# Kernel tuning notes

Hardware: AMD Instinct MI355X
Metric: run time of the kernel (lower is better)

The kernel has to match this reference:

```python
import jax, jax.numpy as jnp
import numpy as np

NUM_PROJS = 7
BLOCK = 256       # HyperAttention block_size
SAMPLE = 256      # HyperAttention sample_size
NUM_HEADS = 16

def _hamming_perm(n):
    a = np.array([0, 1])
    for _ in range(n - 1):
        a = np.concatenate([a, a[::-1] + a.max() + 1])
    return a

_PERM = jnp.asarray(_hamming_perm(NUM_PROJS))           # [128] gray-code-ish bucket reorder
_ENC = (2 ** jnp.arange(NUM_PROJS)).astype(jnp.int32)   # [7]

def _lsh_hash(mat, proj_dir):
    # mat: [B,H,N,d], proj_dir: [d,7] -> bucket ids [B,H,N]
    bits = jnp.einsum('bhnd,dr->bhnr', mat, proj_dir) > 0
    ids = (bits * _ENC).sum(-1)
    return _PERM[ids]

def _attn_lse(q, k, v, scale, bias=None):
    s = jnp.einsum('...qd,...kd->...qk', q, k) * scale
    if bias is not None:
        s = s + bias
    lse = jax.nn.logsumexp(s, axis=-1, keepdims=True)
    o = jnp.einsum('...qk,...kd->...qd', jnp.exp(s - lse), v)
    return o, lse

def _gather(t, idx):
    # gather rows along axis 2: out[b,h,s] = t[b,h,idx[b,h,s]]
    return jnp.take_along_axis(t, idx[..., None], axis=2)

def setup_inputs():
    key = jax.random.key(0)
    ks = jax.random.split(key, 7)
    B, L, D, INNER = 2, 8192, 1024, 1024
    x = jax.random.normal(ks[0], (B, L, D), jnp.float32)
    W_qkv = jax.random.normal(ks[1], (D, 3 * INNER), jnp.float32) / np.sqrt(D)
    b_qkv = jnp.zeros((3 * INNER,), jnp.float32)
    W_proj = jax.random.normal(ks[2], (INNER, D), jnp.float32) / np.sqrt(INNER)
    b_proj = jnp.zeros((D,), jnp.float32)
    proj_dir = jax.random.normal(ks[3], (INNER // NUM_HEADS, NUM_PROJS), jnp.float32)
    sampled_set = jax.random.randint(ks[4], (B, NUM_HEADS, SAMPLE), 0, L)
    return {"x": x, "W_qkv": W_qkv, "b_qkv": b_qkv, "W_proj": W_proj,
            "b_proj": b_proj, "proj_dir": proj_dir, "sampled_set": sampled_set}

def reference(x, W_qkv, b_qkv, W_proj, b_proj, proj_dir, sampled_set):
    B, L, D = x.shape
    qkv = (x @ W_qkv + b_qkv).reshape(B, L, 3, NUM_HEADS, -1).transpose(2, 0, 3, 1, 4)
    q, k, v = qkv[0], qkv[1], qkv[2]                      # [B,H,L,dh]
    dh = q.shape[-1]
    scale = dh ** -0.5
    # 1. sortLSH: stable sort q and k rows by angular-LSH bucket id
    q_idx = jnp.argsort(_lsh_hash(q, proj_dir), axis=2, stable=True)
    k_idx = jnp.argsort(_lsh_hash(k, proj_dir), axis=2, stable=True)
    q_idx_inv = jnp.argsort(q_idx, axis=2, stable=True)   # to restore row order
    qs = _gather(q, q_idx)
    ksort = _gather(k, k_idx)
    vsort = _gather(v, k_idx)
    # block-diagonal exact attention over the sorted order (L % BLOCK == 0 here)
    nb = L // BLOCK
    ab, lb = _attn_lse(qs.reshape(B, NUM_HEADS, nb, BLOCK, dh),
                       ksort.reshape(B, NUM_HEADS, nb, BLOCK, dh),
                       vsort.reshape(B, NUM_HEADS, nb, BLOCK, dh), scale)
    attn_block = ab.reshape(B, NUM_HEADS, L, dh)
    lse_block = lb.reshape(B, NUM_HEADS, L, 1)
    # 2. residual uniformly-sampled attention, masking entries already covered by blocks
    k_sub = _gather(ksort, sampled_set)                   # [B,H,SAMPLE,dh]
    v_sub = _gather(vsort, sampled_set)
    blk_q = jnp.arange(L)[None, None, :, None] // BLOCK   # query block id (query_block_size==BLOCK)
    mask = blk_q == (sampled_set // BLOCK)[:, :, None, :]  # [B,H,L,SAMPLE]
    bias = jnp.where(mask, jnp.finfo(x.dtype).min, 0.0).astype(x.dtype)
    attn_res, lse_res = _attn_lse(qs, k_sub, v_sub, scale, bias)
    lse_res = lse_res + jnp.log(jnp.float32(L) / SAMPLE)  # importance weight n_key/sample_size
    # combine the two attentions via their log-sum-exps
    c = 1.0 / (1.0 + jnp.exp(lse_res - lse_block))
    attn = c * attn_block + (1.0 - c) * attn_res
    out = _gather(attn, q_idx_inv)                        # un-sort rows back to input order
    out = out.transpose(0, 2, 1, 3).reshape(B, L, -1)     # [B,L,inner]
    return out @ W_proj + b_proj
```

## Files before the change

kernel.cpp:

```cpp
#include <hip/hip_runtime.h>
#include <hip/hip_fp16.h>
#include <math.h>


typedef _Float16 f16x8 __attribute__((ext_vector_type(8)));
typedef _Float16 f16x4 __attribute__((ext_vector_type(4)));
typedef float f32x4 __attribute__((ext_vector_type(4)));

#define WLIST_CAP 524288
#define TAU 0.08f

__device__ __forceinline__ void gl_lds16(const void* g, void* s) {
    __builtin_amdgcn_global_load_lds(
        (const __attribute__((address_space(1))) unsigned int*)g,
        (__attribute__((address_space(3))) unsigned int*)s, 16, 0, 0);
}

__global__ __launch_bounds__(256) void fold_kernel(
    const float* __restrict__ W, const float* __restrict__ bias,
    const float* __restrict__ proj, double* __restrict__ fold,
    double* __restrict__ bfold, _Float16* __restrict__ foldh,
    float* __restrict__ bfold32)
{
    int idx = blockIdx.x * 256 + threadIdx.x;
    if (idx < 2 * 16 * 7 * 1024) {
        int task = idx / 7168;
        int rem = idx - task * 7168;
        int i = rem / 7;
        int r = rem - i * 7;
        int h = task & 15, w = task >> 4;
        double s = 0.0;
        const float* wp = W + (size_t)i * 3072 + w * 1024 + h * 64;
        for (int d = 0; d < 64; ++d)
            s += (double)wp[d] * (double)proj[d * 7 + r];
        fold[idx] = s;
        foldh[((size_t)task * 7 + r) * 1024 + i] = (_Float16)s;
    }
    if (idx < 32768)
        foldh[229376 + idx] = (_Float16)0.f;
    if (idx < 224) {
        int r = idx % 7;
        int task = idx / 7;
        int h = task & 15, w = task >> 4;
        double s = 0.0;
        for (int d = 0; d < 64; ++d)
            s += (double)bias[w * 1024 + h * 64 + d] * (double)proj[d * 7 + r];
        bfold[idx] = s;
        bfold32[idx] = (float)s;
    }
}

__global__ __launch_bounds__(256) void hashext_kernel(
    const float* __restrict__ scores, const float* __restrict__ bfold32,
    int* __restrict__ hq, int* __restrict__ hk,
    int* __restrict__ wcount, int* __restrict__ wlist)
{
    int tid = blockIdx.x * 256 + threadIdx.x;
    int row = tid >> 5, task = tid & 31;
    const float* sp = scores + (size_t)row * 256 + task * 7;
    int id = 0, fl = 0;
#pragma unroll
    for (int r = 0; r < 7; ++r) {
        float val = sp[r] + bfold32[task * 7 + r];
        if (fabsf(val) < TAU) fl = 1;
        if (val > 0.f) id |= (1 << r);
    }
    int hsh = id ^ (id >> 1);
    int w = task >> 4, h = task & 15;
    int b = row >> 13, l = row & 8191;
    (w ? hk : hq)[((size_t)(b * 16 + h) << 13) + l] = hsh;
    if (fl) {
        int slot = atomicAdd(wcount, 1);
        if (slot < WLIST_CAP) wlist[slot] = task * 16384 + row;
    }
}

__global__ __launch_bounds__(256) void refine_kernel(
    const float* __restrict__ x, const double* __restrict__ fold,
    const double* __restrict__ bfold, const int* __restrict__ wcount,
    const int* __restrict__ wlist, int* __restrict__ hq, int* __restrict__ hk)
{
    int n = *wcount;
    if (n > WLIST_CAP) n = WLIST_CAP;
    int lane = threadIdx.x & 63;
    int wid = (blockIdx.x * 256 + threadIdx.x) >> 6;
    int nw = gridDim.x * 4;
    for (int e = wid; e < n; e += nw) {
        int code = wlist[e];
        int task = code >> 14, grow = code & 16383;
        const double* f = fold + (size_t)task * 7168;
        const float* xp = x + (size_t)grow * 1024;
        double acc[7] = {0, 0, 0, 0, 0, 0, 0};
        for (int i = lane; i < 1024; i += 64) {
            double xv = (double)xp[i];
#pragma unroll
            for (int rr = 0; rr < 7; ++rr)
                acc[rr] = fma(xv, f[(size_t)i * 7 + rr], acc[rr]);
        }
        int id = 0;
#pragma unroll
        for (int rr = 0; rr < 7; ++rr) {
            double a = acc[rr];
#pragma unroll
            for (int off = 32; off > 0; off >>= 1) a += __shfl_xor(a, off, 64);
            if (a + bfold[task * 7 + rr] > 0.0) id |= (1 << rr);
        }
        if (lane == 0) {
            int hsh = id ^ (id >> 1);
            int w = task >> 4, h = task & 15;
            int b = grow >> 13, l = grow & 8191;
            (w ? hk : hq)[((size_t)(b * 16 + h) << 13) + l] = hsh;
        }
    }
}

__global__ __launch_bounds__(256) void sort_kernel(
    const int* __restrict__ hq, const int* __restrict__ hk,
    int* __restrict__ qidx, int* __restrict__ kidx)
{
    __shared__ unsigned short cnt[128][128];
    __shared__ int tot[128];
    __shared__ int base[128];
    int blk = blockIdx.x;
    int sel = blk >> 5, bh = blk & 31;
    const int* hp = (sel ? hk : hq) + ((size_t)bh << 13);
    int* op = (sel ? kidx : qidx) + ((size_t)bh << 13);
    int t = threadIdx.x;
    for (int i = t; i < 128 * 128 / 2; i += 256) ((unsigned int*)cnt)[i] = 0u;
    __syncthreads();
    if (t < 128) {
        const int* p = hp + t * 64;
        for (int j = 0; j < 64; ++j) cnt[t][p[j]]++;
    }
    __syncthreads();
    if (t < 128) {
        int run = 0;
        for (int c = 0; c < 128; ++c) {
            int x2 = cnt[c][t];
            cnt[c][t] = (unsigned short)run;
            run += x2;
        }
        tot[t] = run;
    }
    __syncthreads();
    if (t == 0) {
        int run = 0;
        for (int v = 0; v < 128; ++v) { base[v] = run; run += tot[v]; }
    }
    __syncthreads();
    if (t < 128) {
        const int* p = hp + t * 64;
        for (int j = 0; j < 64; ++j) {
            int v = p[j];
            int c = cnt[t][v];
            cnt[t][v] = (unsigned short)(c + 1);
            op[base[v] + c] = t * 64 + j;
        }
    }
}

__global__ __launch_bounds__(256) void castx_kernel(
    const float* __restrict__ x, _Float16* __restrict__ xh)
{
    int i = blockIdx.x * 256 + threadIdx.x;
    float4 f = ((const float4*)x)[i];
    _Float16 h4[4] = {(_Float16)f.x, (_Float16)f.y, (_Float16)f.z, (_Float16)f.w};
    *(short4*)&xh[(size_t)i * 4] = *(short4*)h4;
}

__global__ __launch_bounds__(256) void transpose_kernel(
    const float* __restrict__ W, _Float16* __restrict__ Wt, int K, int N)
{
    __shared__ float tile[32][33];
    int bx = blockIdx.x, by = blockIdx.y;
    int tx = threadIdx.x & 31, ty = threadIdx.x >> 5;
    for (int i = ty; i < 32; i += 8)
        tile[i][tx] = W[(size_t)(by * 32 + i) * N + bx * 32 + tx];
    __syncthreads();
    for (int i = ty; i < 32; i += 8)
        Wt[(size_t)(bx * 32 + i) * K + by * 32 + tx] = (_Float16)tile[tx][i];
}

template <int MODE>
__global__ __launch_bounds__(256) void mfma_gemm(
    const _Float16* __restrict__ A, const _Float16* __restrict__ Bt,
    const float* __restrict__ bias, float* __restrict__ C,
    _Float16* __restrict__ Q, _Float16* __restrict__ Kb, _Float16* __restrict__ Vb,
    int K, int N)
{
    __shared__ __align__(16) _Float16 As[128 * 32];
    __shared__ __align__(16) _Float16 Bs[128 * 32];
    int t = threadIdx.x;
    int w = t >> 6, l = t & 63;
    int m0 = blockIdx.y * 128, n0 = blockIdx.x * 128;
    const _Float16* ga = A + (size_t)(m0 + 32 * w + (l >> 2)) * K + (l & 3) * 8;
    const _Float16* gb = Bt + (size_t)(n0 + 32 * w + (l >> 2)) * K + (l & 3) * 8;
    char* lasA = (char*)As + w * 2048;
    char* lasB = (char*)Bs + w * 2048;
    int wr = w >> 1, wc = w & 1;
    int rl = l & 15, ks = l >> 4;
    f32x4 acc[4][4];
#pragma unroll
    for (int m = 0; m < 4; ++m)
#pragma unroll
        for (int n = 0; n < 4; ++n) acc[m][n] = (f32x4){0.f, 0.f, 0.f, 0.f};
    for (int kk = 0; kk < K; kk += 32) {
        __syncthreads();
        gl_lds16(ga, lasA);
        gl_lds16(ga + 16 * K, lasA + 1024);
        gl_lds16(gb, lasB);
        gl_lds16(gb + 16 * K, lasB + 1024);
        ga += 32; gb += 32;
        __syncthreads();
        f16x8 af[4], bf[4];
#pragma unroll
        for (int m = 0; m < 4; ++m)
            af[m] = *(const f16x8*)((char*)As + (64 * wr + 16 * m + rl) * 64 + ks * 16);
#pragma unroll
        for (int n = 0; n < 4; ++n)
            bf[n] = *(const f16x8*)((char*)Bs + (64 * wc + 16 * n + rl) * 64 + ks * 16);
#pragma unroll
        for (int m = 0; m < 4; ++m)
#pragma unroll
            for (int n = 0; n < 4; ++n)
                acc[m][n] = __builtin_amdgcn_mfma_f32_16x16x32_f16(
                    af[m], bf[n], acc[m][n], 0, 0, 0);
    }
#pragma unroll
    for (int m = 0; m < 4; ++m) {
#pragma unroll
        for (int n = 0; n < 4; ++n) {
            int gn = n0 + 64 * wc + 16 * n + rl;
            float bv = (MODE == 2) ? 0.f : bias[gn];
#pragma unroll
            for (int j = 0; j < 4; ++j) {
                int gm = m0 + 64 * wr + 16 * m + 4 * ks + j;
                float val = acc[m][n][j] + bv;
                if (MODE == 1) {
                    int s = gn >> 10, h = (gn >> 6) & 15, d = gn & 63;
                    int b2 = gm >> 13, ll = gm & 8191;
                    _Float16* dst = (s == 0) ? Q : (s == 1 ? Kb : Vb);
                    dst[(((size_t)(b2 * 16 + h) << 13) + ll) * 64 + d] = (_Float16)val;
                } else {
                    C[(size_t)gm * N + gn] = val;
                }
            }
        }
    }
}

__global__ __launch_bounds__(256) void attn_mfma_kernel(
    const _Float16* __restrict__ q, const _Float16* __restrict__ k,
    const _Float16* __restrict__ v, const int* __restrict__ qidx,
    const int* __restrict__ kidx, const int* __restrict__ sampled,
    _Float16* __restrict__ pre)
{
    __shared__ __align__(16) _Float16 Vlds[64 * 64];
    __shared__ int spos[64];
    int bh = blockIdx.x >> 5, qb = blockIdx.x & 31;
    int bb = bh >> 4, hh = bh & 15;
    size_t hb = (size_t)bh << 13;
    int t = threadIdx.x;
    int w = t >> 6, l = t & 63;
    int g = l >> 4, c16 = l & 15;
    int qw0 = qb * 256 + w * 64;
    int orig[4];
    f16x8 qf[4][2];
#pragma unroll
    for (int n = 0; n < 4; ++n) {
        orig[n] = qidx[hb + qw0 + 16 * n + c16];
        const _Float16* qp = q + (hb + orig[n]) * 64 + g * 8;
        qf[n][0] = *(const f16x8*)(qp);
        qf[n][1] = *(const f16x8*)(qp + 32);
    }
    f32x4 o[4][4];
    float mr[4], lr[4];
#pragma unroll
    for (int n = 0; n < 4; ++n) {
        mr[n] = -1e30f; lr[n] = 0.f;
#pragma unroll
        for (int d2 = 0; d2 < 4; ++d2) o[d2][n] = (f32x4){0.f, 0.f, 0.f, 0.f};
    }
    const float LOG32 = 3.4657359027997265f;
    for (int c = 0; c < 8; ++c) {
        bool samp = c >= 4;
        __syncthreads();
        if (t < 64)
            spos[t] = samp ? sampled[(size_t)bh * 256 + (c - 4) * 64 + t]
                           : qb * 256 + c * 64 + t;
        {
            int kk = t >> 2;
            int p = samp ? sampled[(size_t)bh * 256 + (c - 4) * 64 + kk]
                         : qb * 256 + c * 64 + kk;
            int kr = kidx[hb + p];
            const _Float16* vp = v + (hb + kr) * 64;
            int d0 = (t & 3) * 16;
            f16x8 v0 = *(const f16x8*)(vp + d0);
            f16x8 v1 = *(const f16x8*)(vp + d0 + 8);
            int g0 = d0 >> 3;
            *(f16x8*)((char*)Vlds + kk * 128 + (((g0) ^ (kk & 7)) << 4)) = v0;
            *(f16x8*)((char*)Vlds + kk * 128 + (((g0 + 1) ^ (kk & 7)) << 4)) = v1;
        }
        __syncthreads();
        f32x4 sacc[4][4];
#pragma unroll
        for (int m = 0; m < 4; ++m)
#pragma unroll
            for (int n = 0; n < 4; ++n) sacc[m][n] = (f32x4){0.f, 0.f, 0.f, 0.f};
#pragma unroll
        for (int m = 0; m < 4; ++m) {
            int p = spos[16 * m + c16];
            int kr = kidx[hb + p];
            const _Float16* kp = k + (hb + kr) * 64 + g * 8;
            f16x8 kf0 = *(const f16x8*)(kp);
            f16x8 kf1 = *(const f16x8*)(kp + 32);
#pragma unroll
            for (int n = 0; n < 4; ++n)
                sacc[m][n] = __builtin_amdgcn_mfma_f32_16x16x32_f16(
                    kf0, qf[n][0], sacc[m][n], 0, 0, 0);
#pragma unroll
            for (int n = 0; n < 4; ++n)
                sacc[m][n] = __builtin_amdgcn_mfma_f32_16x16x32_f16(
                    kf1, qf[n][1], sacc[m][n], 0, 0, 0);
        }
        f16x4 av[4][4];
#pragma unroll
        for (int m = 0; m < 4; ++m)
#pragma unroll
            for (int d2 = 0; d2 < 4; ++d2) {
                int d = 16 * d2 + c16;
#pragma unroll
                for (int j = 0; j < 4; ++j) {
                    int k2 = 16 * m + 4 * g + j;
                    av[m][d2][j] = *(const _Float16*)((char*)Vlds + k2 * 128 +
                        ((((d >> 3) ^ (k2 & 7)) << 4)) + (d & 7) * 2);
                }
            }
        bool msk[4][4];
#pragma unroll
        for (int m = 0; m < 4; ++m)
#pragma unroll
            for (int r = 0; r < 4; ++r)
                msk[m][r] = samp && ((spos[16 * m + 4 * g + r] >> 8) == qb);
        float badd = samp ? LOG32 : 0.f;
#pragma unroll
        for (int n = 0; n < 4; ++n) {
            float sv[16];
#pragma unroll
            for (int m = 0; m < 4; ++m)
#pragma unroll
                for (int r = 0; r < 4; ++r)
                    sv[4 * m + r] = msk[m][r] ? -1e30f
                                  : sacc[m][n][r] * 0.125f + badd;
            float cm = sv[0];
#pragma unroll
            for (int r = 1; r < 16; ++r) cm = fmaxf(cm, sv[r]);
            cm = fmaxf(cm, __shfl_xor(cm, 16, 64));
            cm = fmaxf(cm, __shfl_xor(cm, 32, 64));
            float nm = fmaxf(mr[n], cm);
            float fq = __expf(mr[n] - nm);
            mr[n] = nm;
            float ps = 0.f;
            float pv16[16];
#pragma unroll
            for (int r = 0; r < 16; ++r) { pv16[r] = __expf(sv[r] - nm); ps += pv16[r]; }
            ps += __shfl_xor(ps, 16, 64);
            ps += __shfl_xor(ps, 32, 64);
            lr[n] = lr[n] * fq + ps;
#pragma unroll
            for (int d2 = 0; d2 < 4; ++d2) {
                o[d2][n][0] *= fq; o[d2][n][1] *= fq;
                o[d2][n][2] *= fq; o[d2][n][3] *= fq;
            }
            f16x4 pb[4];
#pragma unroll
            for (int m = 0; m < 4; ++m) {
                pb[m][0] = (_Float16)pv16[4 * m + 0];
                pb[m][1] = (_Float16)pv16[4 * m + 1];
                pb[m][2] = (_Float16)pv16[4 * m + 2];
                pb[m][3] = (_Float16)pv16[4 * m + 3];
            }
#pragma unroll
            for (int d2 = 0; d2 < 4; ++d2)
#pragma unroll
                for (int m = 0; m < 4; ++m)
                    o[d2][n] = __builtin_amdgcn_mfma_f32_16x16x16f16(
                        av[m][d2], pb[m], o[d2][n], 0, 0, 0);
        }
    }
#pragma unroll
    for (int n = 0; n < 4; ++n) {
        float invl = 1.f / lr[n];
        _Float16* pp = pre + ((size_t)(bb * 8192 + orig[n])) * 1024 + hh * 64;
#pragma unroll
        for (int d2 = 0; d2 < 4; ++d2) {
            f16x4 st;
            st[0] = (_Float16)(o[d2][n][0] * invl);
            st[1] = (_Float16)(o[d2][n][1] * invl);
            st[2] = (_Float16)(o[d2][n][2] * invl);
            st[3] = (_Float16)(o[d2][n][3] * invl);
            *(f16x4*)(pp + 16 * d2 + 4 * g) = st;
        }
    }
}

extern "C" void kernel_launch(void* const* d_in, const int* in_sizes, int n_in,
                              void* d_out, int out_size, void* d_ws, size_t ws_size,
                              hipStream_t stream)
{
    (void)in_sizes; (void)n_in; (void)out_size; (void)ws_size;
    const float* x     = (const float*)d_in[0];
    const float* Wqkv  = (const float*)d_in[1];
    const float* bqkv  = (const float*)d_in[2];
    const float* Wproj = (const float*)d_in[3];
    const float* bproj = (const float*)d_in[4];
    const float* proj  = (const float*)d_in[5];
    const int*   samp  = (const int*)d_in[6];
    float* out = (float*)d_out;

    char* ws = (char*)d_ws;
    size_t off = 0;
    auto take = [&](size_t bytes) {
        char* p = ws + off;
        off = (off + bytes + 255) & ~(size_t)255;
        return p;
    };
    _Float16* xh  = (_Float16*)take(33554432);
    _Float16* q   = (_Float16*)take(33554432);
    _Float16* k   = (_Float16*)take(33554432);
    _Float16* v   = (_Float16*)take(33554432);
    float* scores = (float*)take(16777216);
    _Float16* Wtq = (_Float16*)take(6291456);
    _Float16* Wtp = (_Float16*)take(2097152);
    _Float16* foldh = (_Float16*)take(524288);
    double* fold   = (double*)take(1835008);
    double* bfold  = (double*)take(1792);
    float* bfold32 = (float*)take(896);
    int* wcount = (int*)take(256);
    int* wlist  = (int*)take(WLIST_CAP * 4);
    int* hq   = (int*)take(1048576);
    int* hk   = (int*)take(1048576);
    int* qidx = (int*)take(1048576);
    int* kidx = (int*)take(1048576);
    _Float16* pre = xh;

    hipMemsetAsync(wcount, 0, 4, stream);
    castx_kernel<<<dim3(16384), dim3(256), 0, stream>>>(x, xh);
    fold_kernel<<<dim3(896), dim3(256), 0, stream>>>(
        Wqkv, bqkv, proj, fold, bfold, foldh, bfold32);
    mfma_gemm<2><<<dim3(2, 128), dim3(256), 0, stream>>>(
        xh, foldh, nullptr, scores, nullptr, nullptr, nullptr, 1024, 256);
    hashext_kernel<<<dim3(2048), dim3(256), 0, stream>>>(
        scores, bfold32, hq, hk, wcount, wlist);
    refine_kernel<<<dim3(2048), dim3(256), 0, stream>>>(
        x, fold, bfold, wcount, wlist, hq, hk);
    sort_kernel<<<dim3(64), dim3(256), 0, stream>>>(hq, hk, qidx, kidx);
    transpose_kernel<<<dim3(96, 32), dim3(256), 0, stream>>>(Wqkv, Wtq, 1024, 3072);
    transpose_kernel<<<dim3(32, 32), dim3(256), 0, stream>>>(Wproj, Wtp, 1024, 1024);
    mfma_gemm<1><<<dim3(24, 128), dim3(256), 0, stream>>>(
        xh, Wtq, bqkv, nullptr, q, k, v, 1024, 3072);
    attn_mfma_kernel<<<dim3(1024), dim3(256), 0, stream>>>(
        q, k, v, qidx, kidx, samp, pre);
    mfma_gemm<0><<<dim3(8, 128), dim3(256), 0, stream>>>(
        pre, Wtp, bproj, out, nullptr, nullptr, nullptr, 1024, 1024);
}
```

Baseline: 654.8 us.

## Double-buffer transposed V tiles and prefetch next chunk in attention kernel

The attention kernel now keeps V in a transposed, padded LDS layout with two buffers. The next chunk's key rows, positions and V values are loaded into registers while the current chunk's MFMAs run, which removes one barrier per iteration and allows vectorized f16x4 LDS reads. It also folds the 1/8 score scale into Q in fp16, skips the online-softmax rescale when no row max grows, uses packed RTZ fp16 conversion, and tree-reduces the max and sum. The costs are higher register pressure and doubled LDS, and the RTZ conversion and fp16 pre-scaling change rounding slightly.

```diff
diff --git a/kernel.cpp b/kernel.cpp
--- a/kernel.cpp
+++ b/kernel.cpp
@@ -5,6 +5,7 @@
 
 typedef _Float16 f16x8 __attribute__((ext_vector_type(8)));
 typedef _Float16 f16x4 __attribute__((ext_vector_type(4)));
+typedef __fp16 fp16x2 __attribute__((ext_vector_type(2)));
 typedef float f32x4 __attribute__((ext_vector_type(4)));
 
 #define WLIST_CAP 524288
@@ -255,15 +256,20 @@
     const int* __restrict__ kidx, const int* __restrict__ sampled,
     _Float16* __restrict__ pre)
 {
-    __shared__ __align__(16) _Float16 Vlds[64 * 64];
-    __shared__ int spos[64];
+    __shared__ __align__(16) _Float16 Vt[2][64 * 68];
+    __shared__ int sposS[2][64];
+    __shared__ int krowS[2][64];
     int bh = blockIdx.x >> 5, qb = blockIdx.x & 31;
     int bb = bh >> 4, hh = bh & 15;
     size_t hb = (size_t)bh << 13;
+    size_t bhs = (size_t)bh * 256;
     int t = threadIdx.x;
     int w = t >> 6, l = t & 63;
     int g = l >> 4, c16 = l & 15;
+    int kg = t & 15, dg = t >> 4;
     int qw0 = qb * 256 + w * 64;
+    const _Float16 qs = (_Float16)0.125f;
+
     int orig[4];
     f16x8 qf[4][2];
 #pragma unroll
@@ -272,6 +278,8 @@
         const _Float16* qp = q + (hb + orig[n]) * 64 + g * 8;
         qf[n][0] = *(const f16x8*)(qp);
         qf[n][1] = *(const f16x8*)(qp + 32);
+#pragma unroll
+        for (int j = 0; j < 8; ++j) { qf[n][0][j] *= qs; qf[n][1][j] *= qs; }
     }
     f32x4 o[4][4];
     float mr[4], lr[4];
@@ -282,26 +290,56 @@
         for (int d2 = 0; d2 < 4; ++d2) o[d2][n] = (f32x4){0.f, 0.f, 0.f, 0.f};
     }
     const float LOG32 = 3.4657359027997265f;
+
+    {
+        if (t < 64) {
+            int p = qb * 256 + t;
+            sposS[0][t] = p;
+            krowS[0][t] = kidx[hb + p];
+        }
+        f16x4 vr[4];
+#pragma unroll
+        for (int j2 = 0; j2 < 4; ++j2) {
+            int p = qb * 256 + 4 * kg + j2;
+            int kr = kidx[hb + p];
+            vr[j2] = *(const f16x4*)(v + (hb + kr) * 64 + 4 * dg);
+        }
+#pragma unroll
+        for (int i = 0; i < 4; ++i) {
+            f16x4 o4 = {vr[0][i], vr[1][i], vr[2][i], vr[3][i]};
+            *(f16x4*)&Vt[0][(4 * dg + i) * 68 + 4 * kg] = o4;
+        }
+    }
+
     for (int c = 0; c < 8; ++c) {
+        int cur = c & 1, nxt = cur ^ 1;
         bool samp = c >= 4;
         __syncthreads();
-        if (t < 64)
-            spos[t] = samp ? sampled[(size_t)bh * 256 + (c - 4) * 64 + t]
-                           : qb * 256 + c * 64 + t;
-        {
-            int kk = t >> 2;
-            int p = samp ? sampled[(size_t)bh * 256 + (c - 4) * 64 + kk]
-                         : qb * 256 + c * 64 + kk;
-            int kr = kidx[hb + p];
-            const _Float16* vp = v + (hb + kr) * 64;
-            int d0 = (t & 3) * 16;
-            f16x8 v0 = *(const f16x8*)(vp + d0);
-            f16x8 v1 = *(const f16x8*)(vp + d0 + 8);
-            int g0 = d0 >> 3;
-            *(f16x8*)((char*)Vlds + kk * 128 + (((g0) ^ (kk & 7)) << 4)) = v0;
-            *(f16x8*)((char*)Vlds + kk * 128 + (((g0 + 1) ^ (kk & 7)) << 4)) = v1;
-        }
-        __syncthreads();
+        int krA[4];
+#pragma unroll
+        for (int m = 0; m < 4; ++m) krA[m] = krowS[cur][16 * m + c16];
+        f16x8 kf[4][2];
+#pragma unroll
+        for (int m = 0; m < 4; ++m) {
+            const _Float16* kp = k + (hb + krA[m]) * 64 + g * 8;
+            kf[m][0] = *(const f16x8*)(kp);
+            kf[m][1] = *(const f16x8*)(kp + 32);
+        }
+        int np_s = 0, nkr_s = 0, krn[4];
+        if (c < 7) {
+            bool snx = (c + 1) >= 4;
+            if (t < 64) {
+                np_s = snx ? sampled[bhs + (c - 3) * 64 + t] : qb * 256 + (c + 1) * 64 + t;
+                nkr_s = kidx[hb + np_s];
+            }
+#pragma unroll
+            for (int j2 = 0; j2 < 4; ++j2) {
+                int key = 4 * kg + j2;
+                int p = snx ? sampled[bhs + (c - 3) * 64 + key]
+                            : qb * 256 + (c + 1) * 64 + key;
+                krn[j2] = kidx[hb + p];
+            }
+        }
         f32x4 sacc[4][4];
 #pragma unroll
         for (int m = 0; m < 4; ++m)
@@ -309,76 +347,79 @@
             for (int n = 0; n < 4; ++n) sacc[m][n] = (f32x4){0.f, 0.f, 0.f, 0.f};
 #pragma unroll
         for (int m = 0; m < 4; ++m) {
-            int p = spos[16 * m + c16];
-            int kr = kidx[hb + p];
-            const _Float16* kp = k + (hb + kr) * 64 + g * 8;
-            f16x8 kf0 = *(const f16x8*)(kp);
-            f16x8 kf1 = *(const f16x8*)(kp + 32);
 #pragma unroll
             for (int n = 0; n < 4; ++n)
                 sacc[m][n] = __builtin_amdgcn_mfma_f32_16x16x32_f16(
-                    kf0, qf[n][0], sacc[m][n], 0, 0, 0);
+                    kf[m][0], qf[n][0], sacc[m][n], 0, 0, 0);
 #pragma unroll
             for (int n = 0; n < 4; ++n)
                 sacc[m][n] = __builtin_amdgcn_mfma_f32_16x16x32_f16(
-                    kf1, qf[n][1], sacc[m][n], 0, 0, 0);
+                    kf[m][1], qf[n][1], sacc[m][n], 0, 0, 0);
+        }
+        f16x4 vrn[4];
+        if (c < 7) {
+#pragma unroll
+            for (int j2 = 0; j2 < 4; ++j2)
+                vrn[j2] = *(const f16x4*)(v + (hb + krn[j2]) * 64 + 4 * dg);
         }
         f16x4 av[4][4];
 #pragma unroll
         for (int m = 0; m < 4; ++m)
 #pragma unroll
-            for (int d2 = 0; d2 < 4; ++d2) {
-                int d = 16 * d2 + c16;
-#pragma unroll
-                for (int j = 0; j < 4; ++j) {
-                    int k2 = 16 * m + 4 * g + j;
-                    av[m][d2][j] = *(const _Float16*)((char*)Vlds + k2 * 128 +
-                        ((((d >> 3) ^ (k2 & 7)) << 4)) + (d & 7) * 2);
+            for (int d2 = 0; d2 < 4; ++d2)
+                av[m][d2] = *(const f16x4*)&Vt[cur][(16 * d2 + c16) * 68 + 16 * m + 4 * g];
+        bool msk[4][4];
+#pragma unroll
+        for (int m = 0; m < 4; ++m)
+#pragma unroll
+            for (int r = 0; r < 4; ++r)
+                msk[m][r] = samp && ((sposS[cur][16 * m + 4 * g + r] >> 8) == qb);
+        float badd = samp ? LOG32 : 0.f;
+#pragma unroll
+        for (int n = 0; n < 4; ++n) {
+            float sv[16];
+#pragma unroll
+            for (int m = 0; m < 4; ++m)
+#pragma unroll
+                for (int r = 0; r < 4; ++r)
+                    sv[4 * m + r] = msk[m][r] ? -1e30f : sacc[m][n][r] + badd;
+            float a0 = fmaxf(fmaxf(sv[0], sv[1]), sv[2]);
+            float a1 = fmaxf(fmaxf(sv[3], sv[4]), sv[5]);
+            float a2 = fmaxf(fmaxf(sv[6], sv[7]), sv[8]);
+            float a3 = fmaxf(fmaxf(sv[9], sv[10]), sv[11]);
+            float a4 = fmaxf(fmaxf(sv[12], sv[13]), sv[14]);
+            float cm = fmaxf(fmaxf(fmaxf(a0, a1), a2), fmaxf(fmaxf(a3, a4), sv[15]));
+            cm = fmaxf(cm, __shfl_xor(cm, 16, 64));
+            cm = fmaxf(cm, __shfl_xor(cm, 32, 64));
+            if (__any(cm > mr[n])) {
+                float nm = fmaxf(mr[n], cm);
+                float fq = __expf(mr[n] - nm);
+                mr[n] = nm;
+                lr[n] *= fq;
+#pragma unroll
+                for (int d2 = 0; d2 < 4; ++d2) {
+                    o[d2][n][0] *= fq; o[d2][n][1] *= fq;
+                    o[d2][n][2] *= fq; o[d2][n][3] *= fq;
                 }
             }
-        bool msk[4][4];
-#pragma unroll
-        for (int m = 0; m < 4; ++m)
-#pragma unroll
-            for (int r = 0; r < 4; ++r)
-                msk[m][r] = samp && ((spos[16 * m + 4 * g + r] >> 8) == qb);
-        float badd = samp ? LOG32 : 0.f;
-#pragma unroll
-        for (int n = 0; n < 4; ++n) {
-            float sv[16];
-#pragma unroll
-            for (int m = 0; m < 4; ++m)
-#pragma unroll
-                for (int r = 0; r < 4; ++r)
-                    sv[4 * m + r] = msk[m][r] ? -1e30f
-                                  : sacc[m][n][r] * 0.125f + badd;
-            float cm = sv[0];
-#pragma unroll
-            for (int r = 1; r < 16; ++r) cm = fmaxf(cm, sv[r]);
-            cm = fmaxf(cm, __shfl_xor(cm, 16, 64));
-            cm = fmaxf(cm, __shfl_xor(cm, 32, 64));
-            float nm = fmaxf(mr[n], cm);
-            float fq = __expf(mr[n] - nm);
-            mr[n] = nm;
-            float ps = 0.f;
             float pv16[16];
 #pragma unroll
-            for (int r = 0; r < 16; ++r) { pv16[r] = __expf(sv[r] - nm); ps += pv16[r]; }
+            for (int r = 0; r < 16; ++r) pv16[r] = __expf(sv[r] - mr[n]);
+            float s0 = (pv16[0] + pv16[1]) + (pv16[2] + pv16[3]);
+            float s1 = (pv16[4] + pv16[5]) + (pv16[6] + pv16[7]);
+            float s2 = (pv16[8] + pv16[9]) + (pv16[10] + pv16[11]);
+            float s3 = (pv16[12] + pv16[13]) + (pv16[14] + pv16[15]);
+            float ps = (s0 + s1) + (s2 + s3);
             ps += __shfl_xor(ps, 16, 64);
             ps += __shfl_xor(ps, 32, 64);
-            lr[n] = lr[n] * fq + ps;
-#pragma unroll
-            for (int d2 = 0; d2 < 4; ++d2) {
-                o[d2][n][0] *= fq; o[d2][n][1] *= fq;
-                o[d2][n][2] *= fq; o[d2][n][3] *= fq;
-            }
+            lr[n] += ps;
             f16x4 pb[4];
 #pragma unroll
             for (int m = 0; m < 4; ++m) {
-                pb[m][0] = (_Float16)pv16[4 * m + 0];
-                pb[m][1] = (_Float16)pv16[4 * m + 1];
-                pb[m][2] = (_Float16)pv16[4 * m + 2];
-                pb[m][3] = (_Float16)pv16[4 * m + 3];
+                fp16x2 c0 = __builtin_amdgcn_cvt_pkrtz(pv16[4 * m + 0], pv16[4 * m + 1]);
+                fp16x2 c1 = __builtin_amdgcn_cvt_pkrtz(pv16[4 * m + 2], pv16[4 * m + 3]);
+                pb[m][0] = (_Float16)c0[0]; pb[m][1] = (_Float16)c0[1];
+                pb[m][2] = (_Float16)c1[0]; pb[m][3] = (_Float16)c1[1];
             }
 #pragma unroll
             for (int d2 = 0; d2 < 4; ++d2)
@@ -386,6 +427,14 @@
                 for (int m = 0; m < 4; ++m)
                     o[d2][n] = __builtin_amdgcn_mfma_f32_16x16x16f16(
                         av[m][d2], pb[m], o[d2][n], 0, 0, 0);
+        }
+        if (c < 7) {
+            if (t < 64) { sposS[nxt][t] = np_s; krowS[nxt][t] = nkr_s; }
+#pragma unroll
+            for (int i = 0; i < 4; ++i) {
+                f16x4 o4 = {vrn[0][i], vrn[1][i], vrn[2][i], vrn[3][i]};
+                *(f16x4*)&Vt[nxt][(4 * dg + i) * 68 + 4 * kg] = o4;
+            }
         }
     }
 #pragma unroll
@@ -444,7 +493,7 @@
     int* kidx = (int*)take(1048576);
     _Float16* pre = xh;
 
-    hipMemsetAsync(wcount, 0, 4, stream);
+    (void)hipMemsetAsync(wcount, 0, 4, stream);
     castx_kernel<<<dim3(16384), dim3(256), 0, stream>>>(x, xh);
     fold_kernel<<<dim3(896), dim3(256), 0, stream>>>(
         Wqkv, bqkv, proj, fold, bfold, foldh, bfold32);
```

Measured after the change: 641.7 us. 2.0% less time.
